# Kernel optimization log

Measured on AMD Instinct MI355X. Metric: run time of the kernel, lower is better.

## Reference

```python
import jax, jax.numpy as jnp
import numpy as np

H, C, DK = 4, 63, 64   # n_head, context_size, d_k
NF = H * DK            # n_feat = 256


def setup_inputs() -> dict:
    key = jax.random.key(0)
    ks = jax.random.split(key, 7)
    B, T = 2, 4096
    query = jax.random.normal(ks[0], (B, T, NF), jnp.float32)
    key_t = jax.random.normal(ks[1], (B, T, NF), jnp.float32)   # dummy, unused
    value = jax.random.normal(ks[2], (B, T, NF), jnp.float32)
    mask = jnp.ones((B, 1, T), jnp.bool_)                       # dummy, unused
    s = 1.0 / np.sqrt(NF).astype(np.float32)
    w1 = jax.random.normal(ks[3], (NF, NF), jnp.float32) * s
    w2 = jax.random.normal(ks[4], (H * C, NF), jnp.float32) * s
    w3 = jax.random.normal(ks[5], (NF, NF), jnp.float32) * s
    w_out = jax.random.normal(ks[6], (NF, NF), jnp.float32) * s
    return {"query": query, "key": key_t, "value": value, "mask": mask,
            "w1": w1, "w2": w2, "w3": w3, "w_out": w_out}


def reference(query, key, value, mask, w1, w2, w3, w_out):
    # key and mask are dummies (unused), matching the original module.
    B, T, _ = query.shape
    half = (C - 1) // 2

    q = query @ w1.T                                            # (B,T,NF)
    # synthesized band scores: (B,H,T,C)
    weight = (jax.nn.relu(q) @ w2.T).reshape(B, T, H, C).transpose(0, 2, 1, 3)

    # band geometry: score(i, j) lives at offset k = j - i + half, |j-i| <= half
    j_idx = jnp.arange(T)[:, None] + jnp.arange(C)[None, :] - half   # (T,C)
    valid = (j_idx >= 0) & (j_idx < T)                               # (T,C)
    scores = jnp.where(valid[None, None], weight, -jnp.inf)
    p_attn = jax.nn.softmax(scores, axis=-1)                         # (B,H,T,C)

    v = (value @ w3.T).reshape(B, T, H, DK).transpose(0, 2, 1, 3)    # (B,H,T,DK)
    jc = jnp.clip(j_idx, 0, T - 1)                                   # safe gather idx
    windows = v[:, :, jc, :]                                         # (B,H,T,C,DK)
    x = jnp.einsum('bhtc,bhtcd->bhtd', p_attn, windows)              # (B,H,T,DK)

    x = x.transpose(0, 2, 1, 3).reshape(B, T, NF)
    return x @ w_out.T
```

## Files before the change

kernel.cpp:

```cpp
#include <hip/hip_runtime.h>
#include <hip/hip_bf16.h>
#include <math.h>

typedef _Float16 f16x8 __attribute__((ext_vector_type(8)));
typedef _Float16 f16x4 __attribute__((ext_vector_type(4)));
typedef float    f32x4 __attribute__((ext_vector_type(4)));

__device__ __host__ __forceinline__ int swz(int ch, int row) {
    return (ch & 24) | ((ch & 7) ^ (row & 7));
}
__device__ __forceinline__ f32x4 mfma16(f16x8 a, f16x8 b, f32x4 c) {
    return __builtin_amdgcn_mfma_f32_16x16x32_f16(a, b, c, 0, 0, 0);
}
__device__ __forceinline__ f16x8 cvt8(float4 lo, float4 hi) {
    f16x8 r = { (_Float16)lo.x, (_Float16)lo.y, (_Float16)lo.z, (_Float16)lo.w,
                (_Float16)hi.x, (_Float16)hi.y, (_Float16)hi.z, (_Float16)hi.w };
    return r;
}

__global__ __launch_bounds__(256) void convw(const float* __restrict__ w1,
                                             const float* __restrict__ w2,
                                             const float* __restrict__ w3,
                                             const float* __restrict__ wo,
                                             _Float16* __restrict__ p1,
                                             _Float16* __restrict__ p2,
                                             _Float16* __restrict__ p3,
                                             _Float16* __restrict__ po) {
    int gid = blockIdx.x * 256 + threadIdx.x;
    int widx = gid >> 13;
    int r    = gid & 8191;
    int lane = r & 63;
    int ks   = (r >> 6) & 7;
    int nblk = r >> 9;
    int n  = nblk * 16 + (lane & 15);
    int kc = (ks * 4 + (lane >> 4)) * 8;
    const float* src = widx == 0 ? w1 : widx == 1 ? w2 : widx == 2 ? w3 : wo;
    _Float16*    dst = widx == 0 ? p1 : widx == 1 ? p2 : widx == 2 ? p3 : po;
    f16x8 h = {};
    if (!(widx == 1 && n >= 252)) {
        float4 lo = *(const float4*)&src[n * 256 + kc];
        float4 hi = *(const float4*)&src[n * 256 + kc + 4];
        h = cvt8(lo, hi);
    }
    *(f16x8*)&dst[r * 8] = h;
}

__global__ __launch_bounds__(1024, 4) void mono(const float* __restrict__ query,
                                                const float* __restrict__ value,
                                                const _Float16* __restrict__ w1p,
                                                const _Float16* __restrict__ w2p,
                                                const _Float16* __restrict__ w3p,
                                                const _Float16* __restrict__ wop,
                                                float* __restrict__ outp) {
    __shared__ __align__(16) _Float16 RA[16384];
    __shared__ __align__(16) _Float16 RB[8192];
    __shared__ __align__(16) _Float16 Vs[24576];
    __shared__ __align__(16) _Float16 vwT[26624];

    const int tid = threadIdx.x, lane = tid & 63, wid = tid >> 6;
    const int bidr = blockIdx.x;
    const int work = (bidr & 7) * 32 + (bidr >> 3);
    const int b   = work >> 7;
    const int t0  = (work & 127) * 32;
    const size_t rowb = (size_t)b * 4096;

    _Float16* Aq = RA;
    _Float16* Qr = RA + 8192;
    _Float16* Pl = RA;
    _Float16* sc = RB;
    _Float16* xb = RB;

    {
        int row = tid >> 5, ch = tid & 31;
        const float* qp = &query[(rowb + t0 + row) * 256 + ch * 8];
        float4 qlo = *(const float4*)qp, qhi = *(const float4*)(qp + 4);
        float4 vlo[3], vhi[3];
        #pragma unroll
        for (int it = 0; it < 3; ++it) {
            int slot = it * 1024 + tid;
            int vrow = slot >> 5, vch = slot & 31;
            int jl = t0 - 32 + vrow;
            jl = jl < 0 ? 0 : (jl > 4095 ? 4095 : jl);
            const float* p = &value[(rowb + jl) * 256 + vch * 8];
            vlo[it] = *(const float4*)p;
            vhi[it] = *(const float4*)(p + 4);
        }
        *(f16x8*)&Aq[row * 256 + swz(ch, row) * 8] = cvt8(qlo, qhi);
        #pragma unroll
        for (int it = 0; it < 3; ++it) {
            int slot = it * 1024 + tid;
            int vrow = slot >> 5, vch = slot & 31;
            *(f16x8*)&Vs[vrow * 256 + swz(vch, vrow) * 8] = cvt8(vlo[it], vhi[it]);
        }
    }
    __syncthreads();

    {
        f16x8 bfa[8];
        #pragma unroll
        for (int ks = 0; ks < 8; ++ks)
            bfa[ks] = *(const f16x8*)&w1p[((wid * 8 + ks) * 64 + lane) * 8];
        f32x4 acc[2] = {};
        #pragma unroll
        for (int ks = 0; ks < 8; ++ks) {
            int chn = ks * 4 + (lane >> 4);
            #pragma unroll
            for (int i = 0; i < 2; ++i) {
                int row = i * 16 + (lane & 15);
                f16x8 af = *(const f16x8*)&Aq[row * 256 + swz(chn, row) * 8];
                acc[i] = mfma16(af, bfa[ks], acc[i]);
            }
        }
        const int n = wid * 16 + (lane & 15);
        #pragma unroll
        for (int i = 0; i < 2; ++i)
            #pragma unroll
            for (int r = 0; r < 4; ++r) {
                int row = i * 16 + ((lane >> 4) << 2) + r;
                float v = fmaxf(acc[i][r], 0.f);
                Qr[row * 256 + swz(n >> 3, row) * 8 + (n & 7)] = (_Float16)v;
            }
    }
    __syncthreads();

    {
        f16x8 bfa[8];
        #pragma unroll
        for (int ks = 0; ks < 8; ++ks)
            bfa[ks] = *(const f16x8*)&w2p[((wid * 8 + ks) * 64 + lane) * 8];
        f32x4 acc[2] = {};
        #pragma unroll
        for (int ks = 0; ks < 8; ++ks) {
            int chn = ks * 4 + (lane >> 4);
            #pragma unroll
            for (int i = 0; i < 2; ++i) {
                int row = i * 16 + (lane & 15);
                f16x8 af = *(const f16x8*)&Qr[row * 256 + swz(chn, row) * 8];
                acc[i] = mfma16(af, bfa[ks], acc[i]);
            }
        }
        const int n = wid * 16 + (lane & 15);
        #pragma unroll
        for (int i = 0; i < 2; ++i)
            #pragma unroll
            for (int r = 0; r < 4; ++r) {
                int row = i * 16 + ((lane >> 4) << 2) + r;
                sc[row * 256 + swz(n >> 3, row) * 8 + (n & 7)] = (_Float16)acc[i][r];
            }
    }

    {
        const int rh = wid >> 3, cs = wid & 7;
        f16x8 bfa0[8], bfa1[8];
        #pragma unroll
        for (int ks = 0; ks < 8; ++ks)
            bfa0[ks] = *(const f16x8*)&w3p[(((cs * 2 + 0) * 8 + ks) * 64 + lane) * 8];
        #pragma unroll
        for (int ks = 0; ks < 8; ++ks)
            bfa1[ks] = *(const f16x8*)&w3p[(((cs * 2 + 1) * 8 + ks) * 64 + lane) * 8];
        f32x4 a3[3][2] = {};
        #pragma unroll
        for (int ks = 0; ks < 8; ++ks) {
            int chn = ks * 4 + (lane >> 4);
            #pragma unroll
            for (int mi = 0; mi < 3; ++mi) {
                int row = rh * 48 + mi * 16 + (lane & 15);
                f16x8 af = *(const f16x8*)&Vs[row * 256 + swz(chn, row) * 8];
                a3[mi][0] = mfma16(af, bfa0[ks], a3[mi][0]);
                a3[mi][1] = mfma16(af, bfa1[ks], a3[mi][1]);
            }
        }
        #pragma unroll
        for (int mi = 0; mi < 3; ++mi)
            #pragma unroll
            for (int j = 0; j < 2; ++j) {
                int d  = cs * 32 + j * 16 + (lane & 15);
                int jw = rh * 48 + mi * 16 + ((lane >> 4) << 2);
                f16x4 h = { (_Float16)a3[mi][j][0], (_Float16)a3[mi][j][1],
                            (_Float16)a3[mi][j][2], (_Float16)a3[mi][j][3] };
                *(f16x4*)&vwT[d * 104 + jw] = h;
            }
    }
    __syncthreads();

    const int h = wid >> 2, q = wid & 3;
    #pragma unroll
    for (int it = 0; it < 2; ++it) {
        int s = it * 64 + lane;
        if (s < 104) {
            int rr = h * 32 + q * 8 + s / 13;
            int cc = s % 13;
            f16x8 z = {};
            *(f16x8*)&Pl[rr * 104 + cc * 8] = z;
        }
    }

    {
        const int hf = lane >> 5, c = lane & 31;
        #pragma unroll
        for (int i = 0; i < 4; ++i) {
            int tl = q * 8 + 2 * i + hf;
            int t  = t0 + tl;
            int col0 = h * 63 + c;
            int col1 = col0 + 32;
            int j0 = t + c - 31, j1 = t + c + 1;
            bool ok0 = (j0 >= 0) && (j0 < 4096);
            bool ok1 = (c + 32 < 63) && (j1 >= 0) && (j1 < 4096);
            float s0 = ok0 ? (float)sc[tl * 256 + swz(col0 >> 3, tl) * 8 + (col0 & 7)] : -INFINITY;
            float s1 = ok1 ? (float)sc[tl * 256 + swz(col1 >> 3, tl) * 8 + (col1 & 7)] : -INFINITY;
            float mx = fmaxf(s0, s1);
            #pragma unroll
            for (int off = 16; off > 0; off >>= 1) mx = fmaxf(mx, __shfl_xor(mx, off));
            float e0 = ok0 ? __expf(s0 - mx) : 0.f;
            float e1 = ok1 ? __expf(s1 - mx) : 0.f;
            float sum = e0 + e1;
            #pragma unroll
            for (int off = 16; off > 0; off >>= 1) sum += __shfl_xor(sum, off);
            float inv = 1.0f / sum;
            Pl[(h * 32 + tl) * 104 + (tl + c + 1)] = (_Float16)(e0 * inv);
            if (c + 32 < 63) Pl[(h * 32 + tl) * 104 + (tl + c + 33)] = (_Float16)(e1 * inv);
        }
    }
    __syncthreads();

    {
        const int th = (wid >> 1) & 1, dh = wid & 1;
        f32x4 xa[2] = {};
        #pragma unroll
        for (int ks = 0; ks < 3; ++ks) {
            int chn = ks * 4 + (lane >> 4);
            f16x8 af = *(const f16x8*)&Pl[(h * 32 + th * 16 + (lane & 15)) * 104 + chn * 8];
            #pragma unroll
            for (int j = 0; j < 2; ++j) {
                f16x8 bf = *(const f16x8*)&vwT[(h * 64 + dh * 32 + j * 16 + (lane & 15)) * 104 + chn * 8];
                xa[j] = mfma16(af, bf, xa[j]);
            }
        }
        #pragma unroll
        for (int j = 0; j < 2; ++j)
            #pragma unroll
            for (int r = 0; r < 4; ++r) {
                int row = th * 16 + ((lane >> 4) << 2) + r;
                int n   = h * 64 + dh * 32 + j * 16 + (lane & 15);
                xb[row * 256 + swz(n >> 3, row) * 8 + (n & 7)] = (_Float16)xa[j][r];
            }
    }
    __syncthreads();

    {
        f16x8 bfa[8];
        #pragma unroll
        for (int ks = 0; ks < 8; ++ks)
            bfa[ks] = *(const f16x8*)&wop[((wid * 8 + ks) * 64 + lane) * 8];
        f32x4 oa[2] = {};
        #pragma unroll
        for (int ks = 0; ks < 8; ++ks) {
            int chn = ks * 4 + (lane >> 4);
            #pragma unroll
            for (int i = 0; i < 2; ++i) {
                int row = i * 16 + (lane & 15);
                f16x8 af = *(const f16x8*)&xb[row * 256 + swz(chn, row) * 8];
                oa[i] = mfma16(af, bfa[ks], oa[i]);
            }
        }
        const int n = wid * 16 + (lane & 15);
        #pragma unroll
        for (int i = 0; i < 2; ++i)
            #pragma unroll
            for (int r = 0; r < 4; ++r) {
                int m = t0 + i * 16 + ((lane >> 4) << 2) + r;
                outp[(rowb + m) * 256 + n] = oa[i][r];
            }
    }
}

extern "C" void kernel_launch(void* const* d_in, const int* in_sizes, int n_in,
                              void* d_out, int out_size, void* d_ws, size_t ws_size,
                              hipStream_t stream) {
    const float* query = (const float*)d_in[0];
    const float* value = (const float*)d_in[2];
    const float* w1    = (const float*)d_in[4];
    const float* w2    = (const float*)d_in[5];
    const float* w3    = (const float*)d_in[6];
    const float* w_out = (const float*)d_in[7];

    char* ws = (char*)d_ws;
    _Float16* w1p = (_Float16*)ws;
    _Float16* w2p = w1p + 65536;
    _Float16* w3p = w2p + 65536;
    _Float16* wop = w3p + 65536;

    convw<<<dim3(128), dim3(256), 0, stream>>>(w1, w2, w3, w_out, w1p, w2p, w3p, wop);
    mono<<<dim3(256), dim3(1024), 0, stream>>>(query, value, w1p, w2p, w3p, wop, (float*)d_out);
}
```

Baseline: 24.94 us.

## Halve per-block tile to 16 rows with 512 threads and split V projection

Shrinks each block's tile from 32 to 16 time steps, using 512 threads and 512 blocks instead of 256 blocks of 1024 threads, which cuts shared memory per block. The value window projection is split into two phases: the first 48 rows are computed from the staged window, then the remaining 32 rows, prefetched into registers, are written into the same buffer and projected. The second phase runs alongside the score GEMM. This buffer reuse lets the block fit in less LDS and may raise occupancy. The cost is more redundant value-window loads and projections per output row (80 vs 96 window rows for 16 vs 32 outputs), plus weights reloaded across twice as many blocks.

```diff
diff --git a/kernel.cpp b/kernel.cpp
--- a/kernel.cpp
+++ b/kernel.cpp
@@ -5,6 +5,9 @@
 typedef _Float16 f16x8 __attribute__((ext_vector_type(8)));
 typedef _Float16 f16x4 __attribute__((ext_vector_type(4)));
 typedef float    f32x4 __attribute__((ext_vector_type(4)));
+
+#define PW 96
+#define VW 80
 
 __device__ __host__ __forceinline__ int swz(int ch, int row) {
     return (ch & 24) | ((ch & 7) ^ (row & 7));
@@ -45,31 +48,30 @@
     *(f16x8*)&dst[r * 8] = h;
 }
 
-__global__ __launch_bounds__(1024, 4) void mono(const float* __restrict__ query,
-                                                const float* __restrict__ value,
-                                                const _Float16* __restrict__ w1p,
-                                                const _Float16* __restrict__ w2p,
-                                                const _Float16* __restrict__ w3p,
-                                                const _Float16* __restrict__ wop,
-                                                float* __restrict__ outp) {
-    __shared__ __align__(16) _Float16 RA[16384];
-    __shared__ __align__(16) _Float16 RB[8192];
-    __shared__ __align__(16) _Float16 Vs[24576];
-    __shared__ __align__(16) _Float16 vwT[26624];
+__global__ __launch_bounds__(512, 4) void mono(const float* __restrict__ query,
+                                               const float* __restrict__ value,
+                                               const _Float16* __restrict__ w1p,
+                                               const _Float16* __restrict__ w2p,
+                                               const _Float16* __restrict__ w3p,
+                                               const _Float16* __restrict__ wop,
+                                               float* __restrict__ outp) {
+    __shared__ __align__(16) _Float16 vwT[256 * VW];
+    __shared__ __align__(16) _Float16 VsPl[48 * 256];
+    __shared__ __align__(16) _Float16 Abuf[16 * 256];
+    __shared__ __align__(16) _Float16 Bbuf[16 * 256];
 
     const int tid = threadIdx.x, lane = tid & 63, wid = tid >> 6;
     const int bidr = blockIdx.x;
-    const int work = (bidr & 7) * 32 + (bidr >> 3);
-    const int b   = work >> 7;
-    const int t0  = (work & 127) * 32;
+    const int work = (bidr & 7) * 64 + (bidr >> 3);
+    const int b   = work >> 8;
+    const int t0  = (work & 255) * 16;
     const size_t rowb = (size_t)b * 4096;
 
-    _Float16* Aq = RA;
-    _Float16* Qr = RA + 8192;
-    _Float16* Pl = RA;
-    _Float16* sc = RB;
-    _Float16* xb = RB;
-
+    _Float16* Aq = Abuf;  _Float16* sc = Abuf;
+    _Float16* Qr = Bbuf;  _Float16* xb = Bbuf;
+    _Float16* Vs = VsPl;  _Float16* Pl = VsPl;
+
+    f16x8 vreg0, vreg1;
     {
         int row = tid >> 5, ch = tid & 31;
         const float* qp = &query[(rowb + t0 + row) * 256 + ch * 8];
@@ -77,129 +79,167 @@
         float4 vlo[3], vhi[3];
         #pragma unroll
         for (int it = 0; it < 3; ++it) {
-            int slot = it * 1024 + tid;
+            int slot = it * 512 + tid;
             int vrow = slot >> 5, vch = slot & 31;
             int jl = t0 - 32 + vrow;
             jl = jl < 0 ? 0 : (jl > 4095 ? 4095 : jl);
             const float* p = &value[(rowb + jl) * 256 + vch * 8];
-            vlo[it] = *(const float4*)p;
-            vhi[it] = *(const float4*)(p + 4);
+            vlo[it] = *(const float4*)p;  vhi[it] = *(const float4*)(p + 4);
+        }
+        {
+            int s0 = tid, s1 = 512 + tid;
+            int r0 = s0 >> 5, c0 = s0 & 31, r1 = s1 >> 5, c1 = s1 & 31;
+            int j0 = t0 + 16 + r0;  j0 = j0 > 4095 ? 4095 : j0;
+            int j1 = t0 + 16 + r1;  j1 = j1 > 4095 ? 4095 : j1;
+            const float* p0 = &value[(rowb + j0) * 256 + c0 * 8];
+            const float* p1 = &value[(rowb + j1) * 256 + c1 * 8];
+            vreg0 = cvt8(*(const float4*)p0, *(const float4*)(p0 + 4));
+            vreg1 = cvt8(*(const float4*)p1, *(const float4*)(p1 + 4));
         }
         *(f16x8*)&Aq[row * 256 + swz(ch, row) * 8] = cvt8(qlo, qhi);
         #pragma unroll
         for (int it = 0; it < 3; ++it) {
-            int slot = it * 1024 + tid;
+            int slot = it * 512 + tid;
             int vrow = slot >> 5, vch = slot & 31;
             *(f16x8*)&Vs[vrow * 256 + swz(vch, vrow) * 8] = cvt8(vlo[it], vhi[it]);
         }
     }
     __syncthreads();
 
-    {
+    #pragma unroll
+    for (int j = 0; j < 2; ++j) {
+        const int nblk = wid * 2 + j;
         f16x8 bfa[8];
         #pragma unroll
         for (int ks = 0; ks < 8; ++ks)
-            bfa[ks] = *(const f16x8*)&w1p[((wid * 8 + ks) * 64 + lane) * 8];
+            bfa[ks] = *(const f16x8*)&w3p[((nblk * 8 + ks) * 64 + lane) * 8];
+        f32x4 a3[3] = {};
+        #pragma unroll
+        for (int ks = 0; ks < 8; ++ks) {
+            int chn = ks * 4 + (lane >> 4);
+            #pragma unroll
+            for (int mi = 0; mi < 3; ++mi) {
+                int row = mi * 16 + (lane & 15);
+                f16x8 af = *(const f16x8*)&Vs[row * 256 + swz(chn, row) * 8];
+                a3[mi] = mfma16(af, bfa[ks], a3[mi]);
+            }
+        }
+        const int d = nblk * 16 + (lane & 15);
+        #pragma unroll
+        for (int mi = 0; mi < 3; ++mi) {
+            int jw = mi * 16 + ((lane >> 4) << 2);
+            f16x4 h = { (_Float16)a3[mi][0], (_Float16)a3[mi][1],
+                        (_Float16)a3[mi][2], (_Float16)a3[mi][3] };
+            *(f16x4*)&vwT[d * VW + jw] = h;
+        }
+    }
+    __syncthreads();
+
+    {
+        int r0 = tid >> 5, c0 = tid & 31;
+        *(f16x8*)&Vs[r0 * 256 + swz(c0, r0) * 8] = vreg0;
+        int s1 = 512 + tid;
+        int r1 = s1 >> 5, c1 = s1 & 31;
+        *(f16x8*)&Vs[r1 * 256 + swz(c1, r1) * 8] = vreg1;
+    }
+    {
+        f16x8 bfa0[8], bfa1[8];
+        #pragma unroll
+        for (int ks = 0; ks < 8; ++ks) {
+            bfa0[ks] = *(const f16x8*)&w1p[(((wid * 2 + 0) * 8 + ks) * 64 + lane) * 8];
+            bfa1[ks] = *(const f16x8*)&w1p[(((wid * 2 + 1) * 8 + ks) * 64 + lane) * 8];
+        }
         f32x4 acc[2] = {};
         #pragma unroll
         for (int ks = 0; ks < 8; ++ks) {
             int chn = ks * 4 + (lane >> 4);
-            #pragma unroll
-            for (int i = 0; i < 2; ++i) {
-                int row = i * 16 + (lane & 15);
-                f16x8 af = *(const f16x8*)&Aq[row * 256 + swz(chn, row) * 8];
-                acc[i] = mfma16(af, bfa[ks], acc[i]);
-            }
-        }
-        const int n = wid * 16 + (lane & 15);
-        #pragma unroll
-        for (int i = 0; i < 2; ++i)
+            int row = lane & 15;
+            f16x8 af = *(const f16x8*)&Aq[row * 256 + swz(chn, row) * 8];
+            acc[0] = mfma16(af, bfa0[ks], acc[0]);
+            acc[1] = mfma16(af, bfa1[ks], acc[1]);
+        }
+        #pragma unroll
+        for (int j = 0; j < 2; ++j)
             #pragma unroll
             for (int r = 0; r < 4; ++r) {
-                int row = i * 16 + ((lane >> 4) << 2) + r;
-                float v = fmaxf(acc[i][r], 0.f);
+                int row = ((lane >> 4) << 2) + r;
+                int n   = wid * 32 + j * 16 + (lane & 15);
+                float v = fmaxf(acc[j][r], 0.f);
                 Qr[row * 256 + swz(n >> 3, row) * 8 + (n & 7)] = (_Float16)v;
             }
     }
     __syncthreads();
 
-    {
+    #pragma unroll
+    for (int j = 0; j < 2; ++j) {
+        const int nblk = wid * 2 + j;
         f16x8 bfa[8];
         #pragma unroll
         for (int ks = 0; ks < 8; ++ks)
-            bfa[ks] = *(const f16x8*)&w2p[((wid * 8 + ks) * 64 + lane) * 8];
+            bfa[ks] = *(const f16x8*)&w3p[((nblk * 8 + ks) * 64 + lane) * 8];
+        f32x4 a3[2] = {};
+        #pragma unroll
+        for (int ks = 0; ks < 8; ++ks) {
+            int chn = ks * 4 + (lane >> 4);
+            #pragma unroll
+            for (int mi = 0; mi < 2; ++mi) {
+                int row = mi * 16 + (lane & 15);
+                f16x8 af = *(const f16x8*)&Vs[row * 256 + swz(chn, row) * 8];
+                a3[mi] = mfma16(af, bfa[ks], a3[mi]);
+            }
+        }
+        const int d = nblk * 16 + (lane & 15);
+        #pragma unroll
+        for (int mi = 0; mi < 2; ++mi) {
+            int jw = 48 + mi * 16 + ((lane >> 4) << 2);
+            f16x4 h = { (_Float16)a3[mi][0], (_Float16)a3[mi][1],
+                        (_Float16)a3[mi][2], (_Float16)a3[mi][3] };
+            *(f16x4*)&vwT[d * VW + jw] = h;
+        }
+    }
+    {
+        f16x8 bfa0[8], bfa1[8];
+        #pragma unroll
+        for (int ks = 0; ks < 8; ++ks) {
+            bfa0[ks] = *(const f16x8*)&w2p[(((wid * 2 + 0) * 8 + ks) * 64 + lane) * 8];
+            bfa1[ks] = *(const f16x8*)&w2p[(((wid * 2 + 1) * 8 + ks) * 64 + lane) * 8];
+        }
         f32x4 acc[2] = {};
         #pragma unroll
         for (int ks = 0; ks < 8; ++ks) {
             int chn = ks * 4 + (lane >> 4);
-            #pragma unroll
-            for (int i = 0; i < 2; ++i) {
-                int row = i * 16 + (lane & 15);
-                f16x8 af = *(const f16x8*)&Qr[row * 256 + swz(chn, row) * 8];
-                acc[i] = mfma16(af, bfa[ks], acc[i]);
-            }
-        }
-        const int n = wid * 16 + (lane & 15);
-        #pragma unroll
-        for (int i = 0; i < 2; ++i)
+            int row = lane & 15;
+            f16x8 af = *(const f16x8*)&Qr[row * 256 + swz(chn, row) * 8];
+            acc[0] = mfma16(af, bfa0[ks], acc[0]);
+            acc[1] = mfma16(af, bfa1[ks], acc[1]);
+        }
+        #pragma unroll
+        for (int j = 0; j < 2; ++j)
             #pragma unroll
             for (int r = 0; r < 4; ++r) {
-                int row = i * 16 + ((lane >> 4) << 2) + r;
-                sc[row * 256 + swz(n >> 3, row) * 8 + (n & 7)] = (_Float16)acc[i][r];
-            }
-    }
-
-    {
-        const int rh = wid >> 3, cs = wid & 7;
-        f16x8 bfa0[8], bfa1[8];
-        #pragma unroll
-        for (int ks = 0; ks < 8; ++ks)
-            bfa0[ks] = *(const f16x8*)&w3p[(((cs * 2 + 0) * 8 + ks) * 64 + lane) * 8];
-        #pragma unroll
-        for (int ks = 0; ks < 8; ++ks)
-            bfa1[ks] = *(const f16x8*)&w3p[(((cs * 2 + 1) * 8 + ks) * 64 + lane) * 8];
-        f32x4 a3[3][2] = {};
-        #pragma unroll
-        for (int ks = 0; ks < 8; ++ks) {
-            int chn = ks * 4 + (lane >> 4);
-            #pragma unroll
-            for (int mi = 0; mi < 3; ++mi) {
-                int row = rh * 48 + mi * 16 + (lane & 15);
-                f16x8 af = *(const f16x8*)&Vs[row * 256 + swz(chn, row) * 8];
-                a3[mi][0] = mfma16(af, bfa0[ks], a3[mi][0]);
-                a3[mi][1] = mfma16(af, bfa1[ks], a3[mi][1]);
-            }
-        }
-        #pragma unroll
-        for (int mi = 0; mi < 3; ++mi)
-            #pragma unroll
-            for (int j = 0; j < 2; ++j) {
-                int d  = cs * 32 + j * 16 + (lane & 15);
-                int jw = rh * 48 + mi * 16 + ((lane >> 4) << 2);
-                f16x4 h = { (_Float16)a3[mi][j][0], (_Float16)a3[mi][j][1],
-                            (_Float16)a3[mi][j][2], (_Float16)a3[mi][j][3] };
-                *(f16x4*)&vwT[d * 104 + jw] = h;
-            }
-    }
-    __syncthreads();
-
-    const int h = wid >> 2, q = wid & 3;
+                int row = ((lane >> 4) << 2) + r;
+                int n   = wid * 32 + j * 16 + (lane & 15);
+                sc[row * 256 + swz(n >> 3, row) * 8 + (n & 7)] = (_Float16)acc[j][r];
+            }
+    }
+    __syncthreads();
+
+    const int h = wid >> 1, q8 = (wid & 1) * 8;
     #pragma unroll
     for (int it = 0; it < 2; ++it) {
         int s = it * 64 + lane;
-        if (s < 104) {
-            int rr = h * 32 + q * 8 + s / 13;
-            int cc = s % 13;
+        if (s < 96) {
+            int rr = h * 16 + q8 + s / 12;
+            int cc = s % 12;
             f16x8 z = {};
-            *(f16x8*)&Pl[rr * 104 + cc * 8] = z;
-        }
-    }
-
+            *(f16x8*)&Pl[rr * PW + cc * 8] = z;
+        }
+    }
     {
         const int hf = lane >> 5, c = lane & 31;
         #pragma unroll
         for (int i = 0; i < 4; ++i) {
-            int tl = q * 8 + 2 * i + hf;
+            int tl = q8 + 2 * i + hf;
             int t  = t0 + tl;
             int col0 = h * 63 + c;
             int col1 = col0 + 32;
@@ -217,22 +257,22 @@
             #pragma unroll
             for (int off = 16; off > 0; off >>= 1) sum += __shfl_xor(sum, off);
             float inv = 1.0f / sum;
-            Pl[(h * 32 + tl) * 104 + (tl + c + 1)] = (_Float16)(e0 * inv);
-            if (c + 32 < 63) Pl[(h * 32 + tl) * 104 + (tl + c + 33)] = (_Float16)(e1 * inv);
-        }
-    }
-    __syncthreads();
-
-    {
-        const int th = (wid >> 1) & 1, dh = wid & 1;
+            Pl[(h * 16 + tl) * PW + (tl + c + 1)] = (_Float16)(e0 * inv);
+            if (c + 32 < 63) Pl[(h * 16 + tl) * PW + (tl + c + 33)] = (_Float16)(e1 * inv);
+        }
+    }
+    __syncthreads();
+
+    {
+        const int h2 = wid >> 1, dh = wid & 1;
         f32x4 xa[2] = {};
         #pragma unroll
         for (int ks = 0; ks < 3; ++ks) {
             int chn = ks * 4 + (lane >> 4);
-            f16x8 af = *(const f16x8*)&Pl[(h * 32 + th * 16 + (lane & 15)) * 104 + chn * 8];
+            f16x8 af = *(const f16x8*)&Pl[(h2 * 16 + (lane & 15)) * PW + chn * 8];
             #pragma unroll
             for (int j = 0; j < 2; ++j) {
-                f16x8 bf = *(const f16x8*)&vwT[(h * 64 + dh * 32 + j * 16 + (lane & 15)) * 104 + chn * 8];
+                f16x8 bf = *(const f16x8*)&vwT[(h2 * 64 + dh * 32 + j * 16 + (lane & 15)) * VW + chn * 8];
                 xa[j] = mfma16(af, bf, xa[j]);
             }
         }
@@ -240,36 +280,36 @@
         for (int j = 0; j < 2; ++j)
             #pragma unroll
             for (int r = 0; r < 4; ++r) {
-                int row = th * 16 + ((lane >> 4) << 2) + r;
-                int n   = h * 64 + dh * 32 + j * 16 + (lane & 15);
+                int row = ((lane >> 4) << 2) + r;
+                int n   = h2 * 64 + dh * 32 + j * 16 + (lane & 15);
                 xb[row * 256 + swz(n >> 3, row) * 8 + (n & 7)] = (_Float16)xa[j][r];
             }
     }
     __syncthreads();
 
     {
-        f16x8 bfa[8];
-        #pragma unroll
-        for (int ks = 0; ks < 8; ++ks)
-            bfa[ks] = *(const f16x8*)&wop[((wid * 8 + ks) * 64 + lane) * 8];
-        f32x4 oa[2] = {};
-        #pragma unroll
-        for (int ks = 0; ks < 8; ++ks) {
-            int chn = ks * 4 + (lane >> 4);
-            #pragma unroll
-            for (int i = 0; i < 2; ++i) {
-                int row = i * 16 + (lane & 15);
-                f16x8 af = *(const f16x8*)&xb[row * 256 + swz(chn, row) * 8];
-                oa[i] = mfma16(af, bfa[ks], oa[i]);
-            }
-        }
-        const int n = wid * 16 + (lane & 15);
-        #pragma unroll
-        for (int i = 0; i < 2; ++i)
+        f16x8 bfa0[8], bfa1[8];
+        #pragma unroll
+        for (int ks = 0; ks < 8; ++ks) {
+            bfa0[ks] = *(const f16x8*)&wop[(((wid * 2 + 0) * 8 + ks) * 64 + lane) * 8];
+            bfa1[ks] = *(const f16x8*)&wop[(((wid * 2 + 1) * 8 + ks) * 64 + lane) * 8];
+        }
+        f32x4 acc[2] = {};
+        #pragma unroll
+        for (int ks = 0; ks < 8; ++ks) {
+            int chn = ks * 4 + (lane >> 4);
+            int row = lane & 15;
+            f16x8 af = *(const f16x8*)&xb[row * 256 + swz(chn, row) * 8];
+            acc[0] = mfma16(af, bfa0[ks], acc[0]);
+            acc[1] = mfma16(af, bfa1[ks], acc[1]);
+        }
+        #pragma unroll
+        for (int j = 0; j < 2; ++j)
             #pragma unroll
             for (int r = 0; r < 4; ++r) {
-                int m = t0 + i * 16 + ((lane >> 4) << 2) + r;
-                outp[(rowb + m) * 256 + n] = oa[i][r];
+                int m = t0 + ((lane >> 4) << 2) + r;
+                int n = wid * 32 + j * 16 + (lane & 15);
+                outp[(rowb + m) * 256 + n] = acc[j][r];
             }
     }
 }
@@ -291,5 +331,5 @@
     _Float16* wop = w3p + 65536;
 
     convw<<<dim3(128), dim3(256), 0, stream>>>(w1, w2, w3, w_out, w1p, w2p, w3p, wop);
-    mono<<<dim3(256), dim3(1024), 0, stream>>>(query, value, w1p, w2p, w3p, wop, (float*)d_out);
-}
+    mono<<<dim3(512), dim3(512), 0, stream>>>(query, value, w1p, w2p, w3p, wop, (float*)d_out);
+}
```

New measurement: 28.93 us. 1.16x slower.
